# Kernel optimization log

Measured on AMD Instinct MI355X. Metric: run time of the kernel, lower is better.

## Reference

```python
import jax, jax.numpy as jnp
import numpy as np

N = 50000      # num_nodes
R = 8          # num_relations
H = 128        # hidden_channels
C = 40         # num_classes
E = 800000     # num_edges


def _seg_mean_over_relations(msgs, dst, etype):
    """Per-relation mean aggregation (PyG RGCNConv aggr='mean'), summed over relations.
    msgs: [E, H] per-edge messages; dst: [E] target nodes; etype: [E] relation ids.
    Returns [N, H].
    """
    seg = dst * R + etype                                   # [E] combined (node, relation) id
    sums = jax.ops.segment_sum(msgs, seg, num_segments=N * R)          # [N*R, H]
    cnt = jax.ops.segment_sum(jnp.ones((msgs.shape[0], 1), msgs.dtype), seg,
                              num_segments=N * R)                       # [N*R, 1]
    mean = sums / jnp.maximum(cnt, 1.0)
    return mean.reshape(N, R, -1).sum(axis=1)               # [N, H]


def setup_inputs() -> dict:
    key = jax.random.key(0)
    ks = jax.random.split(key, 10)
    s = 0.02
    edge_index = jax.random.randint(ks[0], (2, E), 0, N, dtype=jnp.int32)
    edge_type = jax.random.randint(ks[1], (E,), 0, R, dtype=jnp.int32)
    return {
        "edge_index": edge_index,
        "edge_type": edge_type,
        "W1": jax.random.normal(ks[2], (R, N, H), jnp.float32) * s,    # featureless: embedding per (rel, node)
        "root1": jax.random.normal(ks[3], (N, H), jnp.float32) * s,    # root embedding (x=None)
        "b1": jnp.zeros((H,), jnp.float32),
        "W2": jax.random.normal(ks[4], (R, H, H), jnp.float32) * s,
        "root2": jax.random.normal(ks[5], (H, H), jnp.float32) * s,
        "b2": jnp.zeros((H,), jnp.float32),
        "lin_w": jax.random.normal(ks[6], (H, C), jnp.float32) * s,
        "lin_b": jnp.zeros((C,), jnp.float32),
    }


def reference(edge_index, edge_type, W1, root1, b1, W2, root2, b2, lin_w, lin_b):
    src, dst = edge_index[0], edge_index[1]  # flow: source_to_target

    # ---- layer 1 (featureless RGCNConv): gather relation-specific node embeddings ----
    msgs1 = W1[edge_type, src]                               # [E, H]
    h = _seg_mean_over_relations(msgs1, dst, edge_type)      # [N, H]
    h = h + root1 + b1
    h = jax.nn.relu(h)

    # ---- layer 2: relation-specific dense transform then gather-scatter ----
    xr = jnp.einsum('nh,rhk->rnk', h, W2)                    # [R, N, H]
    msgs2 = xr[edge_type, src]                               # [E, H]
    h2 = _seg_mean_over_relations(msgs2, dst, edge_type)     # [N, H]
    h2 = h2 + h @ root2 + b2
    h2 = jax.nn.relu(h2)

    # ---- final linear ----
    return h2 @ lin_w + lin_b                                # [N, C]
```

## Files before the change

### kernel.cpp

```cpp
#include <hip/hip_runtime.h>

#define HH 128
#define RNUM 8
#define CC 40
#define SCAN_BLK 4096
#define LDA 136
#define SRCMASK 0x7FFFFFF

typedef __attribute__((ext_vector_type(8))) short short8;
typedef __attribute__((ext_vector_type(4))) float floatx4;

__device__ __forceinline__ float bf2f(unsigned short u) {
    union { unsigned u; float f; } c;
    c.u = ((unsigned)u) << 16;
    return c.f;
}
__device__ __forceinline__ unsigned short f2bf(float f) {
    union { float f; unsigned u; } c;
    c.f = f;
    return (unsigned short)((c.u + 0x7FFFu + ((c.u >> 16) & 1u)) >> 16);
}


__global__ void count_kernel(const int* __restrict__ dst, const int* __restrict__ et,
                             int* __restrict__ cnt, int E) {
    int e = blockIdx.x * blockDim.x + threadIdx.x;
    if (e < E) atomicAdd(&cnt[dst[e] * RNUM + et[e]], 1);
}

__global__ void scan1_kernel(const int* __restrict__ cnt, int* __restrict__ off,
                             int* __restrict__ bsum, int n) {
    __shared__ int ts[256];
    int t = threadIdx.x;
    int start = blockIdx.x * SCAN_BLK + t * 16;
    int v[16];
    int s = 0;
#pragma unroll
    for (int j = 0; j < 16; ++j) {
        int idx = start + j;
        v[j] = (idx < n) ? cnt[idx] : 0;
        s += v[j];
    }
    ts[t] = s;
    __syncthreads();
    for (int ofs = 1; ofs < 256; ofs <<= 1) {
        int y = (t >= ofs) ? ts[t - ofs] : 0;
        __syncthreads();
        ts[t] += y;
        __syncthreads();
    }
    int run = ts[t] - s;
    if (t == 255) bsum[blockIdx.x] = ts[255];
#pragma unroll
    for (int j = 0; j < 16; ++j) {
        int idx = start + j;
        if (idx < n) off[idx] = run;
        run += v[j];
    }
}

__global__ void scan2_kernel(int* __restrict__ bsum, int nb) {
    __shared__ int ts[256];
    int t = threadIdx.x;
    int v = (t < nb) ? bsum[t] : 0;
    ts[t] = v;
    __syncthreads();
    for (int ofs = 1; ofs < 256; ofs <<= 1) {
        int y = (t >= ofs) ? ts[t - ofs] : 0;
        __syncthreads();
        ts[t] += y;
        __syncthreads();
    }
    if (t < nb) bsum[t] = ts[t] - v;
}

__global__ void scan3_kernel(int* __restrict__ off, int* __restrict__ cur,
                             const int* __restrict__ bsum, int n, int E) {
    int i = blockIdx.x * blockDim.x + threadIdx.x;
    if (i < n) {
        int o = off[i] + bsum[i >> 12];
        off[i] = o;
        cur[i] = o;
    }
    if (i == 0) off[n] = E;
}

__global__ void invc_kernel(const int* __restrict__ off, float* __restrict__ invc, int n) {
    int i = blockIdx.x * blockDim.x + threadIdx.x;
    if (i < n) invc[i] = 1.0f / fmaxf(1.0f, (float)(off[i + 1] - off[i]));
}

__global__ void fill_kernel(const int* __restrict__ src, const int* __restrict__ dst,
                            const int* __restrict__ et, int* __restrict__ cur,
                            int* __restrict__ elist, int E) {
    int e = blockIdx.x * blockDim.x + threadIdx.x;
    if (e < E) {
        int key = dst[e] * RNUM + et[e];
        int p = atomicAdd(&cur[key], 1);
        elist[p] = (int)(((unsigned)et[e] << 27) | (unsigned)src[e]);
    }
}

__global__ void gather1_kernel(const int* __restrict__ off, const int* __restrict__ elist,
                               const float* __restrict__ invc, const float* __restrict__ W1,
                               const float* __restrict__ root1, const float* __restrict__ b1,
                               unsigned short* __restrict__ hbf, int Nn) {
    int w = (blockIdx.x * blockDim.x + threadIdx.x) >> 6;
    if (w >= Nn) return;
    int lane = threadIdx.x & 63;
    int qid = lane >> 4, cl = lane & 15;
    int b = off[w * 8], e = off[w * 8 + 8];

    float s0[8] = {0.f, 0.f, 0.f, 0.f, 0.f, 0.f, 0.f, 0.f};
    float s1[8] = {0.f, 0.f, 0.f, 0.f, 0.f, 0.f, 0.f, 0.f};

#define EDGE1(IDX, S)                                                             \
    {                                                                             \
        unsigned pk = (unsigned)elist[IDX];                                       \
        int rr = pk >> 27;                                                        \
        int ss = pk & SRCMASK;                                                    \
        float wt = invc[w * 8 + rr];                                              \
        const float* p = W1 + ((size_t)rr * Nn + ss) * HH + cl * 8;               \
        float4 v0 = *(const float4*)p;                                            \
        float4 v1 = *(const float4*)(p + 4);                                      \
        S[0] += v0.x * wt; S[1] += v0.y * wt; S[2] += v0.z * wt; S[3] += v0.w * wt; \
        S[4] += v1.x * wt; S[5] += v1.y * wt; S[6] += v1.z * wt; S[7] += v1.w * wt; \
    }

    int i = b + qid;
    for (; i + 4 < e; i += 8) {
        EDGE1(i, s0);
        EDGE1(i + 4, s1);
    }
    if (i < e) EDGE1(i, s0);
#undef EDGE1

#pragma unroll
    for (int k = 0; k < 8; ++k) {
        s0[k] += s1[k];
        s0[k] += __shfl_xor(s0[k], 16);
        s0[k] += __shfl_xor(s0[k], 32);
    }

    if (qid == 0) {
        const float* rp = root1 + (size_t)w * HH + cl * 8;
        float4 r0 = *(const float4*)rp;
        float4 r1 = *(const float4*)(rp + 4);
        float4 c0 = *(const float4*)(b1 + cl * 8);
        float4 c1 = *(const float4*)(b1 + cl * 8 + 4);
        float o[8];
        o[0] = fmaxf(s0[0] + r0.x + c0.x, 0.f); o[1] = fmaxf(s0[1] + r0.y + c0.y, 0.f);
        o[2] = fmaxf(s0[2] + r0.z + c0.z, 0.f); o[3] = fmaxf(s0[3] + r0.w + c0.w, 0.f);
        o[4] = fmaxf(s0[4] + r1.x + c1.x, 0.f); o[5] = fmaxf(s0[5] + r1.y + c1.y, 0.f);
        o[6] = fmaxf(s0[6] + r1.z + c1.z, 0.f); o[7] = fmaxf(s0[7] + r1.w + c1.w, 0.f);
        ushort4 pk0, pk1;
        pk0.x = f2bf(o[0]); pk0.y = f2bf(o[1]); pk0.z = f2bf(o[2]); pk0.w = f2bf(o[3]);
        pk1.x = f2bf(o[4]); pk1.y = f2bf(o[5]); pk1.z = f2bf(o[6]); pk1.w = f2bf(o[7]);
        unsigned short* hp = hbf + (size_t)w * HH + cl * 8;
        *(ushort4*)hp = pk0;
        *(ushort4*)(hp + 4) = pk1;
    }
}

__global__ void agg_kernel(const int* __restrict__ off, const int* __restrict__ elist,
                           const float* __restrict__ invc, const unsigned short* __restrict__ hbf,
                           unsigned short* __restrict__ aggr, int Nn) {
    int w = (blockIdx.x * blockDim.x + threadIdx.x) >> 6;
    if (w >= Nn) return;
    int lane = threadIdx.x & 63;
    int qid = lane >> 4, cl = lane & 15;

    int o[9];
#pragma unroll
    for (int k = 0; k < 9; ++k) o[k] = off[w * 8 + k];

#pragma unroll
    for (int r = 0; r < RNUM; ++r) {
        int b = o[r], e = o[r + 1];
        float s[8] = {0.f, 0.f, 0.f, 0.f, 0.f, 0.f, 0.f, 0.f};
        for (int i = b + qid; i < e; i += 4) {
            int ss = elist[i] & SRCMASK;
            const unsigned short* hp = hbf + (size_t)ss * HH + cl * 8;
            ushort4 v0 = *(const ushort4*)hp;
            ushort4 v1 = *(const ushort4*)(hp + 4);
            s[0] += bf2f(v0.x); s[1] += bf2f(v0.y); s[2] += bf2f(v0.z); s[3] += bf2f(v0.w);
            s[4] += bf2f(v1.x); s[5] += bf2f(v1.y); s[6] += bf2f(v1.z); s[7] += bf2f(v1.w);
        }
#pragma unroll
        for (int k = 0; k < 8; ++k) {
            s[k] += __shfl_xor(s[k], 16);
            s[k] += __shfl_xor(s[k], 32);
        }
        if (qid == 0) {
            float wt = invc[w * 8 + r];
            ushort4 p0, p1;
            p0.x = f2bf(s[0] * wt); p0.y = f2bf(s[1] * wt);
            p0.z = f2bf(s[2] * wt); p0.w = f2bf(s[3] * wt);
            p1.x = f2bf(s[4] * wt); p1.y = f2bf(s[5] * wt);
            p1.z = f2bf(s[6] * wt); p1.w = f2bf(s[7] * wt);
            unsigned short* ap = aggr + ((size_t)w * RNUM + r) * HH + cl * 8;
            *(ushort4*)ap = p0;
            *(ushort4*)(ap + 4) = p1;
        }
    }
}

__global__ void tcast_kernel(const float* __restrict__ root2, const float* __restrict__ W2,
                             unsigned short* __restrict__ Bt) {
    int bid = blockIdx.x;
    int c = bid >> 5;
    int id = (bid & 31) * 256 + threadIdx.x;
    int n = id >> 6, kp = id & 63;
    const float* B = (c == 0) ? root2 : W2 + (size_t)(c - 1) * HH * HH;
    float f0 = B[(2 * kp) * HH + n];
    float f1 = B[(2 * kp + 1) * HH + n];
    unsigned v = (unsigned)f2bf(f0) | ((unsigned)f2bf(f1) << 16);
    *(unsigned*)(Bt + (size_t)c * HH * HH + n * HH + 2 * kp) = v;
}

__global__ __launch_bounds__(256, 3) void gemm9_kernel(
    const unsigned short* __restrict__ hbf, const unsigned short* __restrict__ aggr,
    const unsigned short* __restrict__ Bt, const float* __restrict__ b2,
    const float* __restrict__ lin_w, const float* __restrict__ lin_b,
    float* __restrict__ out, int Nn) {
    __shared__ unsigned short As[64 * LDA];
    __shared__ unsigned short Bs[128 * LDA];
    const int tid = threadIdx.x;
    const int lane = tid & 63, wv = tid >> 6;
    const int quad = lane >> 4, l16 = lane & 15;
    const int mr = wv & 1, nc = wv >> 1;
    const int m0 = blockIdx.x * 64;

    floatx4 acc[2][4];
#pragma unroll
    for (int a = 0; a < 2; ++a)
#pragma unroll
        for (int bb = 0; bb < 4; ++bb) acc[a][bb] = (floatx4){0.f, 0.f, 0.f, 0.f};

    for (int c = 0; c < 9; ++c) {
        __syncthreads();
        const unsigned short* Bsrc = Bt + (size_t)c * HH * HH;
#pragma unroll
        for (int it = 0; it < 8; ++it) {
            int id = tid + it * 256;
            int rw = id >> 4, c8 = id & 15;
            *(uint4*)(Bs + rw * LDA + c8 * 8) = *(const uint4*)(Bsrc + rw * HH + c8 * 8);
        }
#pragma unroll
        for (int it = 0; it < 4; ++it) {
            int id = tid + it * 256;
            int rw = id >> 4, c8 = id & 15;
            uint4 v = make_uint4(0, 0, 0, 0);
            if (m0 + rw < Nn) {
                const unsigned short* Asrc =
                    (c == 0) ? (hbf + (size_t)(m0 + rw) * HH)
                             : (aggr + ((size_t)(m0 + rw) * RNUM + (c - 1)) * HH);
                v = *(const uint4*)(Asrc + c8 * 8);
            }
            *(uint4*)(As + rw * LDA + c8 * 8) = v;
        }
        __syncthreads();
#pragma unroll
        for (int ks = 0; ks < 4; ++ks) {
            short8 a0 = *(const short8*)(As + (mr * 32 + l16) * LDA + ks * 32 + quad * 8);
            short8 a1 = *(const short8*)(As + (mr * 32 + 16 + l16) * LDA + ks * 32 + quad * 8);
#pragma unroll
            for (int nf = 0; nf < 4; ++nf) {
                short8 b = *(const short8*)(Bs + (nc * 64 + nf * 16 + l16) * LDA + ks * 32 + quad * 8);
                acc[0][nf] = __builtin_amdgcn_mfma_f32_16x16x32_bf16(a0, b, acc[0][nf], 0, 0, 0);
                acc[1][nf] = __builtin_amdgcn_mfma_f32_16x16x32_bf16(a1, b, acc[1][nf], 0, 0, 0);
            }
        }
    }

    __syncthreads();
#pragma unroll
    for (int mf = 0; mf < 2; ++mf)
#pragma unroll
        for (int nf = 0; nf < 4; ++nf) {
            int gcol = nc * 64 + nf * 16 + l16;
            float bb = b2[gcol];
#pragma unroll
            for (int rg = 0; rg < 4; ++rg) {
                int row = mr * 32 + mf * 16 + quad * 4 + rg;
                float v = fmaxf(acc[mf][nf][rg] + bb, 0.f);
                As[row * LDA + gcol] = f2bf(v);
            }
        }
    for (int it = 0; it < 20; ++it) {
        int id = tid + it * 256;
        int n = id >> 7, k = id & 127;
        Bs[n * LDA + k] = f2bf(lin_w[k * CC + n]);
    }
    __syncthreads();

    floatx4 acc2[3];
#pragma unroll
    for (int nf = 0; nf < 3; ++nf) acc2[nf] = (floatx4){0.f, 0.f, 0.f, 0.f};
#pragma unroll
    for (int ks = 0; ks < 4; ++ks) {
        short8 a = *(const short8*)(As + (wv * 16 + l16) * LDA + ks * 32 + quad * 8);
#pragma unroll
        for (int nf = 0; nf < 3; ++nf) {
            short8 b = *(const short8*)(Bs + (nf * 16 + l16) * LDA + ks * 32 + quad * 8);
            acc2[nf] = __builtin_amdgcn_mfma_f32_16x16x32_bf16(a, b, acc2[nf], 0, 0, 0);
        }
    }
#pragma unroll
    for (int nf = 0; nf < 3; ++nf) {
        int col = nf * 16 + l16;
        if (col < CC) {
            float lb = lin_b[col];
#pragma unroll
            for (int rg = 0; rg < 4; ++rg) {
                int grow = m0 + wv * 16 + quad * 4 + rg;
                if (grow < Nn) out[(size_t)grow * CC + col] = acc2[nf][rg] + lb;
            }
        }
    }
}


extern "C" void kernel_launch(void* const* d_in, const int* in_sizes, int n_in,
                              void* d_out, int out_size, void* d_ws, size_t ws_size,
                              hipStream_t stream) {
    const int* ei      = (const int*)d_in[0];
    const int* et      = (const int*)d_in[1];
    const float* W1    = (const float*)d_in[2];
    const float* root1 = (const float*)d_in[3];
    const float* b1    = (const float*)d_in[4];
    const float* W2    = (const float*)d_in[5];
    const float* root2 = (const float*)d_in[6];
    const float* b2    = (const float*)d_in[7];
    const float* lw    = (const float*)d_in[8];
    const float* lb    = (const float*)d_in[9];
    float* out = (float*)d_out;

    const int E = in_sizes[1];
    const int N = in_sizes[3] / HH;
    const int NR = N * RNUM;
    const int NB = (NR + SCAN_BLK - 1) / SCAN_BLK;

    int* off   = (int*)d_ws;
    int* cur   = off + (NR + 1);
    int* bsum  = cur + NR;
    int* elist = bsum + 256;
    float* invc = (float*)(elist + E);
    size_t iofs = (size_t)(NR + 1) + NR + 256 + E + NR;
    iofs = (iofs + 3) & ~(size_t)3;
    unsigned short* hbf  = (unsigned short*)((int*)d_ws + iofs);
    unsigned short* Bt   = hbf + (size_t)N * HH;
    unsigned short* aggr = Bt + (size_t)9 * HH * HH;

    const int* src = ei;
    const int* dst = ei + E;

    hipMemsetAsync(cur, 0, (size_t)NR * sizeof(int), stream);
    count_kernel<<<(E + 255) / 256, 256, 0, stream>>>(dst, et, cur, E);
    scan1_kernel<<<NB, 256, 0, stream>>>(cur, off, bsum, NR);
    scan2_kernel<<<1, 256, 0, stream>>>(bsum, NB);
    scan3_kernel<<<(NR + 255) / 256, 256, 0, stream>>>(off, cur, bsum, NR, E);
    invc_kernel<<<(NR + 255) / 256, 256, 0, stream>>>(off, invc, NR);
    fill_kernel<<<(E + 255) / 256, 256, 0, stream>>>(src, dst, et, cur, elist, E);

    tcast_kernel<<<9 * 32, 256, 0, stream>>>(root2, W2, Bt);

    const int gblocks = (N * 64 + 255) / 256;
    gather1_kernel<<<gblocks, 256, 0, stream>>>(off, elist, invc, W1, root1, b1, hbf, N);
    agg_kernel<<<gblocks, 256, 0, stream>>>(off, elist, invc, hbf, aggr, N);
    gemm9_kernel<<<(N + 63) / 64, 256, 0, stream>>>(hbf, aggr, Bt, b2, lw, lb, out, N);
}
```

Measured before the change: 571.0 us.

## Remap agg to one 16-lane group per (node,relation) and fuse invc into scan

The aggregation kernel now gives each (node, relation) segment its own 16-thread group instead of looping over 8 relations inside a wavefront. Each group uses 16-byte bf16 loads and two accumulator sets, which removes the cross-quarter shuffle reduction and the idle lanes on short segments. The inverse-count computation is folded into scan3 using the raw counts, which drops one kernel launch. gather1 is unrolled to four independent accumulators for more memory-level parallelism, at the cost of more registers.

```diff
diff --git a/kernel.cpp b/kernel.cpp
--- a/kernel.cpp
+++ b/kernel.cpp
@@ -13,6 +13,11 @@
 __device__ __forceinline__ float bf2f(unsigned short u) {
     union { unsigned u; float f; } c;
     c.u = ((unsigned)u) << 16;
+    return c.f;
+}
+__device__ __forceinline__ float u2f(unsigned u) {
+    union { unsigned u; float f; } c;
+    c.u = u;
     return c.f;
 }
 __device__ __forceinline__ unsigned short f2bf(float f) {
@@ -75,19 +80,17 @@
 }
 
 __global__ void scan3_kernel(int* __restrict__ off, int* __restrict__ cur,
-                             const int* __restrict__ bsum, int n, int E) {
+                             const int* __restrict__ bsum, float* __restrict__ invc,
+                             int n, int E) {
     int i = blockIdx.x * blockDim.x + threadIdx.x;
     if (i < n) {
+        int c = cur[i];
+        invc[i] = 1.0f / fmaxf(1.0f, (float)c);
         int o = off[i] + bsum[i >> 12];
         off[i] = o;
         cur[i] = o;
     }
     if (i == 0) off[n] = E;
-}
-
-__global__ void invc_kernel(const int* __restrict__ off, float* __restrict__ invc, int n) {
-    int i = blockIdx.x * blockDim.x + threadIdx.x;
-    if (i < n) invc[i] = 1.0f / fmaxf(1.0f, (float)(off[i + 1] - off[i]));
 }
 
 __global__ void fill_kernel(const int* __restrict__ src, const int* __restrict__ dst,
@@ -113,6 +116,8 @@
 
     float s0[8] = {0.f, 0.f, 0.f, 0.f, 0.f, 0.f, 0.f, 0.f};
     float s1[8] = {0.f, 0.f, 0.f, 0.f, 0.f, 0.f, 0.f, 0.f};
+    float s2[8] = {0.f, 0.f, 0.f, 0.f, 0.f, 0.f, 0.f, 0.f};
+    float s3[8] = {0.f, 0.f, 0.f, 0.f, 0.f, 0.f, 0.f, 0.f};
 
 #define EDGE1(IDX, S)                                                             \
     {                                                                             \
@@ -128,16 +133,18 @@
     }
 
     int i = b + qid;
-    for (; i + 4 < e; i += 8) {
+    for (; i + 12 < e; i += 16) {
         EDGE1(i, s0);
         EDGE1(i + 4, s1);
-    }
-    if (i < e) EDGE1(i, s0);
+        EDGE1(i + 8, s2);
+        EDGE1(i + 12, s3);
+    }
+    for (; i < e; i += 4) EDGE1(i, s0);
 #undef EDGE1
 
 #pragma unroll
     for (int k = 0; k < 8; ++k) {
-        s0[k] += s1[k];
+        s0[k] += s1[k] + s2[k] + s3[k];
         s0[k] += __shfl_xor(s0[k], 16);
         s0[k] += __shfl_xor(s0[k], 32);
     }
@@ -164,45 +171,49 @@
 
 __global__ void agg_kernel(const int* __restrict__ off, const int* __restrict__ elist,
                            const float* __restrict__ invc, const unsigned short* __restrict__ hbf,
-                           unsigned short* __restrict__ aggr, int Nn) {
-    int w = (blockIdx.x * blockDim.x + threadIdx.x) >> 6;
-    if (w >= Nn) return;
-    int lane = threadIdx.x & 63;
-    int qid = lane >> 4, cl = lane & 15;
-
-    int o[9];
-#pragma unroll
-    for (int k = 0; k < 9; ++k) o[k] = off[w * 8 + k];
-
-#pragma unroll
-    for (int r = 0; r < RNUM; ++r) {
-        int b = o[r], e = o[r + 1];
-        float s[8] = {0.f, 0.f, 0.f, 0.f, 0.f, 0.f, 0.f, 0.f};
-        for (int i = b + qid; i < e; i += 4) {
-            int ss = elist[i] & SRCMASK;
-            const unsigned short* hp = hbf + (size_t)ss * HH + cl * 8;
-            ushort4 v0 = *(const ushort4*)hp;
-            ushort4 v1 = *(const ushort4*)(hp + 4);
-            s[0] += bf2f(v0.x); s[1] += bf2f(v0.y); s[2] += bf2f(v0.z); s[3] += bf2f(v0.w);
-            s[4] += bf2f(v1.x); s[5] += bf2f(v1.y); s[6] += bf2f(v1.z); s[7] += bf2f(v1.w);
-        }
-#pragma unroll
-        for (int k = 0; k < 8; ++k) {
-            s[k] += __shfl_xor(s[k], 16);
-            s[k] += __shfl_xor(s[k], 32);
-        }
-        if (qid == 0) {
-            float wt = invc[w * 8 + r];
-            ushort4 p0, p1;
-            p0.x = f2bf(s[0] * wt); p0.y = f2bf(s[1] * wt);
-            p0.z = f2bf(s[2] * wt); p0.w = f2bf(s[3] * wt);
-            p1.x = f2bf(s[4] * wt); p1.y = f2bf(s[5] * wt);
-            p1.z = f2bf(s[6] * wt); p1.w = f2bf(s[7] * wt);
-            unsigned short* ap = aggr + ((size_t)w * RNUM + r) * HH + cl * 8;
-            *(ushort4*)ap = p0;
-            *(ushort4*)(ap + 4) = p1;
-        }
-    }
+                           unsigned short* __restrict__ aggr, int NQ) {
+    int g = blockIdx.x * blockDim.x + threadIdx.x;
+    int q = g >> 4;
+    if (q >= NQ) return;
+    int cl = g & 15;
+    int b = off[q], e = off[q + 1];
+    float wt = invc[q];
+
+    float sa[8] = {0.f, 0.f, 0.f, 0.f, 0.f, 0.f, 0.f, 0.f};
+    float sb[8] = {0.f, 0.f, 0.f, 0.f, 0.f, 0.f, 0.f, 0.f};
+
+#define ACC8(V, S)                                                 \
+    {                                                              \
+        S[0] += u2f(V.x << 16); S[1] += u2f(V.x & 0xFFFF0000u);    \
+        S[2] += u2f(V.y << 16); S[3] += u2f(V.y & 0xFFFF0000u);    \
+        S[4] += u2f(V.z << 16); S[5] += u2f(V.z & 0xFFFF0000u);    \
+        S[6] += u2f(V.w << 16); S[7] += u2f(V.w & 0xFFFF0000u);    \
+    }
+
+    int i = b;
+    for (; i + 1 < e; i += 2) {
+        int t0 = elist[i] & SRCMASK;
+        int t1 = elist[i + 1] & SRCMASK;
+        uint4 v0 = *(const uint4*)(hbf + (size_t)t0 * HH + cl * 8);
+        uint4 v1 = *(const uint4*)(hbf + (size_t)t1 * HH + cl * 8);
+        ACC8(v0, sa);
+        ACC8(v1, sb);
+    }
+    if (i < e) {
+        int t0 = elist[i] & SRCMASK;
+        uint4 v0 = *(const uint4*)(hbf + (size_t)t0 * HH + cl * 8);
+        ACC8(v0, sa);
+    }
+#undef ACC8
+
+    ushort4 p0, p1;
+    p0.x = f2bf((sa[0] + sb[0]) * wt); p0.y = f2bf((sa[1] + sb[1]) * wt);
+    p0.z = f2bf((sa[2] + sb[2]) * wt); p0.w = f2bf((sa[3] + sb[3]) * wt);
+    p1.x = f2bf((sa[4] + sb[4]) * wt); p1.y = f2bf((sa[5] + sb[5]) * wt);
+    p1.z = f2bf((sa[6] + sb[6]) * wt); p1.w = f2bf((sa[7] + sb[7]) * wt);
+    unsigned short* ap = aggr + (size_t)q * HH + cl * 8;
+    *(ushort4*)ap = p0;
+    *(ushort4*)(ap + 4) = p1;
 }
 
 __global__ void tcast_kernel(const float* __restrict__ root2, const float* __restrict__ W2,
@@ -359,14 +370,12 @@
     count_kernel<<<(E + 255) / 256, 256, 0, stream>>>(dst, et, cur, E);
     scan1_kernel<<<NB, 256, 0, stream>>>(cur, off, bsum, NR);
     scan2_kernel<<<1, 256, 0, stream>>>(bsum, NB);
-    scan3_kernel<<<(NR + 255) / 256, 256, 0, stream>>>(off, cur, bsum, NR, E);
-    invc_kernel<<<(NR + 255) / 256, 256, 0, stream>>>(off, invc, NR);
+    scan3_kernel<<<(NR + 255) / 256, 256, 0, stream>>>(off, cur, bsum, invc, NR, E);
     fill_kernel<<<(E + 255) / 256, 256, 0, stream>>>(src, dst, et, cur, elist, E);
 
     tcast_kernel<<<9 * 32, 256, 0, stream>>>(root2, W2, Bt);
 
-    const int gblocks = (N * 64 + 255) / 256;
-    gather1_kernel<<<gblocks, 256, 0, stream>>>(off, elist, invc, W1, root1, b1, hbf, N);
-    agg_kernel<<<gblocks, 256, 0, stream>>>(off, elist, invc, hbf, aggr, N);
+    gather1_kernel<<<(N * 64 + 255) / 256, 256, 0, stream>>>(off, elist, invc, W1, root1, b1, hbf, N);
+    agg_kernel<<<(NR * 16 + 255) / 256, 256, 0, stream>>>(off, elist, invc, hbf, aggr, NR);
     gemm9_kernel<<<(N + 63) / 64, 256, 0, stream>>>(hbf, aggr, Bt, b2, lw, lb, out, N);
 }
```

Result: faster. 544.9 us (-4.6%).
